# Optimization experiments

Hardware: AMD Instinct MI355X
Metric: run time of the kernel (lower is better)

## Reference

```python
import jax, jax.numpy as jnp
import numpy as np

C = 256  # in_channels
B, N = 8, 2048


def setup_inputs() -> dict:
    key = jax.random.key(0)
    ks = jax.random.split(key, 9)
    s = 1.0 / np.sqrt(C)  # conv1d default init scale (approx)
    return {
        "x": jax.random.normal(ks[0], (B, C, N), jnp.float32),
        "wq": jax.random.normal(ks[1], (C, C), jnp.float32) * s,
        "bq": jax.random.normal(ks[2], (C,), jnp.float32) * s,
        "wk": jax.random.normal(ks[3], (C, C), jnp.float32) * s,
        "bk": jax.random.normal(ks[4], (C,), jnp.float32) * s,
        "wv": jax.random.normal(ks[5], (C, C), jnp.float32) * s,
        "bv": jax.random.normal(ks[6], (C,), jnp.float32) * s,
        "wo": jax.random.normal(ks[7], (C, C), jnp.float32) * s,
        "bo": jax.random.normal(ks[8], (C,), jnp.float32) * s,
    }


def reference(x, wq, bq, wk, bk, wv, bv, wo, bo):
    # 1x1 Conv1d == channel-wise linear: [C_out,C_in] x [B,C_in,N] -> [B,C_out,N]
    proj = lambda w, b, t: jnp.einsum('ci,bin->bcn', w, t) + b[None, :, None]
    q = proj(wq, bq, x)
    k = proj(wk, bk, x)
    v = proj(wv, bv, x)
    norm = 1.0 / (x.shape[1] ** 0.5)
    # scores: w[b,n,m] = sum_c q[b,c,n] k[b,c,m]
    w = jnp.einsum('bcn,bcm->bnm', q, k) * norm
    w = jax.nn.softmax(w, axis=2)
    # attn output: sum_m v[b,c,m] w[b,n,m] -> [B,C,N]
    av = jnp.einsum('bcm,bnm->bcn', v, w)
    out = proj(wo, bo, av)
    return x + out
```

## Files before the change

### kernel.cpp

```cpp
#include <hip/hip_runtime.h>
#include <hip/hip_bf16.h>

#define CCH 256
#define NSEQ 2048
#define BATCH 8

typedef __hip_bfloat16 bf16;
typedef short s8v __attribute__((ext_vector_type(8)));
typedef float f4v __attribute__((ext_vector_type(4)));
typedef float f16v __attribute__((ext_vector_type(16)));

struct __align__(8) bf16x4 { bf16 v[4]; };

__device__ __forceinline__ float b2f(bf16 h) { return __bfloat162float(h); }
__device__ __forceinline__ bf16 f2b(float f) { return __float2bfloat16(f); }

#define MFMA16(a, b, c) __builtin_amdgcn_mfma_f32_16x16x32_bf16((a), (b), (c), 0, 0, 0)
#define MFMA32(a, b, c) __builtin_amdgcn_mfma_f32_32x32x16_bf16((a), (b), (c), 0, 0, 0)

__device__ __forceinline__ void gload_lds16(const bf16* g, bf16* l) {
    __builtin_amdgcn_global_load_lds(
        (const __attribute__((address_space(1))) unsigned int*)(g),
        (__attribute__((address_space(3))) unsigned int*)(l), 16, 0, 0);
}

__global__ __launch_bounds__(256) void prepw_kernel(
    const float* __restrict__ wq, const float* __restrict__ wk,
    const float* __restrict__ wv, const float* __restrict__ wo,
    bf16* __restrict__ wqb, bf16* __restrict__ wkb,
    bf16* __restrict__ wvb, bf16* __restrict__ wob)
{
    int base = (blockIdx.x * 256 + threadIdx.x) * 8;
    int mat = base >> 16, off = base & 65535;
    const float* s = (mat == 0) ? wq : (mat == 1) ? wk : (mat == 2) ? wv : wo;
    bf16* d = (mat == 0) ? wqb : (mat == 1) ? wkb : (mat == 2) ? wvb : wob;
    int doff = (mat == 3) ? off : (off ^ (((off >> 8) & 7) << 3));
    bf16 tmp[8];
    #pragma unroll
    for (int j = 0; j < 8; ++j) tmp[j] = f2b(s[off + j]);
    *(s8v*)&d[doff] = *(const s8v*)tmp;
}

__global__ __launch_bounds__(512, 6) void qkvprep_kernel(
    const float* __restrict__ x,
    const bf16* __restrict__ Wq, const bf16* __restrict__ Wk,
    const bf16* __restrict__ Wv,
    const float* __restrict__ bq, const float* __restrict__ bk,
    const float* __restrict__ bv,
    bf16* __restrict__ qTt, bf16* __restrict__ kTt, bf16* __restrict__ Vt)
{
    __shared__ bf16 xs[64][260];
    __shared__ bf16 wbuf[2][2][4096];

    const int tile = blockIdx.x;
    const int flat0 = tile * 64;
    const int phase = blockIdx.y;
    const int b = flat0 >> 11, nn = flat0 & 2047;
    const int tid = threadIdx.x;
    const int w = tid >> 6, lane = tid & 63;
    const int l15 = lane & 15, quad = lane >> 4;
    const int ng = w & 3;
    const int ch = w >> 2;
    const float* xb = x + (size_t)b * CCH * NSEQ;

    bf16* qt = qTt + (size_t)tile * 16384;
    bf16* kt = kTt + (size_t)tile * 16384;
    bf16* Vtb = Vt + (size_t)b * CCH * NSEQ;

    const bf16* Wm = (phase == 0) ? Wq : (phase == 1) ? Wk : Wv;
    auto stage = [&](int j, int par) {
        const bf16* src = Wm + (size_t)(ch * 8 + j) * 4096;
        bf16* dst = &wbuf[ch][par][0];
        int seg = (w & 3) * 2;
        gload_lds16(src + (seg + 0) * 512 + lane * 8, dst + (seg + 0) * 512);
        gload_lds16(src + (seg + 1) * 512 + lane * 8, dst + (seg + 1) * 512);
    };

    stage(0, 0);
    #pragma unroll
    for (int i = 0; i < 8; ++i) {
        int f4i = i * 512 + tid;
        int c = f4i >> 4, nq = f4i & 15;
        float4 v4 = *(const float4*)&xb[(size_t)c * NSEQ + nn + nq * 4];
        xs[nq * 4 + 0][c] = f2b(v4.x);
        xs[nq * 4 + 1][c] = f2b(v4.y);
        xs[nq * 4 + 2][c] = f2b(v4.z);
        xs[nq * 4 + 3][c] = f2b(v4.w);
    }
    __syncthreads();

    s8v xf[8];
    #pragma unroll
    for (int t = 0; t < 8; ++t)
        xf[t] = *(const s8v*)&xs[ng * 16 + l15][t * 32 + quad * 8];

    int par = 0;
    #pragma unroll
    for (int j = 0; j < 8; ++j) {
        if (j < 7) stage(j + 1, par ^ 1);

        const char* wb = (const char*)&wbuf[ch][par][0];
        s8v wf[8];
        #pragma unroll
        for (int t = 0; t < 8; ++t)
            wf[t] = *(const s8v*)(wb + l15 * 512 +
                                  ((t * 64 + quad * 16) ^ ((l15 & 7) << 4)));

        const int cs = ch * 8 + j;
        if (phase < 2) {
            f4v a0 = {}, a1 = {};
            #pragma unroll
            for (int t = 0; t < 4; ++t) {
                a0 = MFMA16(wf[t], xf[t], a0);
                a1 = MFMA16(wf[t + 4], xf[t + 4], a1);
            }
            const bool isq = (phase == 0);
            const float* bm = isq ? bq : bk;
            bf16* ot = isq ? qt : kt;
            const float sc = isq ? 0.0625f : 1.0f;
            float4 bb4 = *(const float4*)&bm[cs * 16 + quad * 4];
            float bbr[4] = { bb4.x, bb4.y, bb4.z, bb4.w };
            bf16x4 pk;
            #pragma unroll
            for (int r = 0; r < 4; ++r)
                pk.v[r] = f2b((a0[r] + a1[r] + bbr[r]) * sc);
            int nl = ng * 16 + l15;
            *(bf16x4*)&ot[(cs * 2 + (quad >> 1)) * 512 + nl * 8 + (quad & 1) * 4] = pk;
        } else {
            f4v a0 = {}, a1 = {};
            #pragma unroll
            for (int t = 0; t < 4; ++t) {
                a0 = MFMA16(xf[t], wf[t], a0);
                a1 = MFMA16(xf[t + 4], wf[t + 4], a1);
            }
            int c = cs * 16 + l15;
            float bb = bv[c];
            bf16x4 pk;
            #pragma unroll
            for (int r = 0; r < 4; ++r)
                pk.v[r] = f2b(a0[r] + a1[r] + bb);
            const int m16 = (nn >> 4) + ng;
            size_t e0 = ((size_t)m16 * 256 + c) * 16 + (quad >> 1) * 8 + (quad & 1) * 4;
            *(bf16x4*)&Vtb[e0] = pk;
        }
        __syncthreads();
        par ^= 1;
    }
}

__global__ __launch_bounds__(256, 2) void flash_kernel(
    const bf16* __restrict__ qTt, const bf16* __restrict__ kTt,
    const bf16* __restrict__ Vt, bf16* __restrict__ Opart,
    float* __restrict__ lpart)
{
    __shared__ bf16 Kc[16384];
    __shared__ bf16 Ps[64][68];
    __shared__ float l_s[2][64];

    const int b = blockIdx.x, nt = blockIdx.y, ms = blockIdx.z;
    const int tid = threadIdx.x;
    const int W = tid >> 6, lane = tid & 63;
    const int l31 = lane & 31, h = lane >> 5;
    const int ng = W >> 1, mg = W & 1;
    const int mb = ms * 16;
    const bf16* Vtb = Vt + (size_t)b * CCH * NSEQ;

    s8v qf[16];
    {
        const bf16* qt = qTt + (size_t)(b * 32 + nt) * 16384;
        #pragma unroll
        for (int t = 0; t < 16; ++t)
            qf[t] = *(const s8v*)&qt[(t * 2 + h) * 512 + (ng * 32 + l31) * 8];
    }
    const bf16* vbase = Vtb + (size_t)(W * 64 + l31) * 16 + h * 8;

    f16v O[2][2] = {};
    float lsum = 0.f;

    auto stageK = [&](int a) {
        const bf16* kt = kTt + (size_t)(b * 32 + a) * 16384;
        #pragma unroll
        for (int i = 0; i < 8; ++i) {
            int ch = W * 8 + i;
            gload_lds16(kt + ch * 512 + lane * 8, &Kc[ch * 512]);
        }
    };

    stageK(mb);
    __syncthreads();

    for (int mt = 0; mt < 16; ++mt) {
        f16v S0 = {}, S1 = {};
        __builtin_amdgcn_s_setprio(1);
        #pragma unroll
        for (int t = 0; t < 8; ++t) {
            s8v kf0 = *(const s8v*)&Kc[(t * 2 + h) * 512 + (mg * 32 + l31) * 8];
            s8v kf1 = *(const s8v*)&Kc[((t + 8) * 2 + h) * 512 + (mg * 32 + l31) * 8];
            S0 = MFMA32(kf0, qf[t], S0);
            S1 = MFMA32(kf1, qf[t + 8], S1);
        }
        __builtin_amdgcn_s_setprio(0);
        s8v vf[2][4];
        #pragma unroll
        for (int ks = 0; ks < 4; ++ks)
            #pragma unroll
            for (int cr = 0; cr < 2; ++cr)
                vf[cr][ks] = *(const s8v*)(vbase
                    + (size_t)((mb + mt) * 4 + ks) * 4096 + cr * 512);
        #pragma unroll
        for (int q = 0; q < 4; ++q) {
            bf16x4 pk;
            #pragma unroll
            for (int r = 0; r < 4; ++r) {
                float e = __expf(fminf(S0[q * 4 + r] + S1[q * 4 + r], 60.f));
                lsum += e;
                pk.v[r] = f2b(e);
            }
            *(bf16x4*)&Ps[ng * 32 + l31][mg * 32 + q * 8 + h * 4] = pk;
        }
        __syncthreads();

        if (mt < 15) stageK(mb + mt + 1);

        __builtin_amdgcn_s_setprio(1);
        #pragma unroll
        for (int ks = 0; ks < 4; ++ks) {
            s8v pf0 = *(const s8v*)&Ps[l31][ks * 16 + h * 8];
            s8v pf1 = *(const s8v*)&Ps[32 + l31][ks * 16 + h * 8];
            O[0][0] = MFMA32(vf[0][ks], pf0, O[0][0]);
            O[0][1] = MFMA32(vf[0][ks], pf1, O[0][1]);
            O[1][0] = MFMA32(vf[1][ks], pf0, O[1][0]);
            O[1][1] = MFMA32(vf[1][ks], pf1, O[1][1]);
        }
        __builtin_amdgcn_s_setprio(0);
        __syncthreads();
    }

    {
        float s = lsum + __shfl_xor(lsum, 32);
        if (h == 0) l_s[mg][ng * 32 + l31] = s;
    }
    __syncthreads();
    const size_t pb = (size_t)(b * 32 + nt) * 2 + ms;
    if (tid < 64) lpart[pb * 64 + tid] = l_s[0][tid] + l_s[1][tid];

    bf16* Ob = Opart + pb * 16384;
    #pragma unroll
    for (int cr = 0; cr < 2; ++cr)
        #pragma unroll
        for (int g2 = 0; g2 < 2; ++g2) {
            int n = g2 * 32 + l31;
            #pragma unroll
            for (int q2 = 0; q2 < 4; ++q2) {
                bf16x4 pk;
                #pragma unroll
                for (int j = 0; j < 4; ++j) pk.v[j] = f2b(O[cr][g2][q2 * 4 + j]);
                int c = W * 64 + cr * 32 + q2 * 8 + 4 * h;
                *(bf16x4*)&Ob[(size_t)n * 256 + c] = pk;
            }
        }
}

__global__ __launch_bounds__(512, 4) void outproj_kernel(
    const bf16* __restrict__ Opart, const float* __restrict__ lpart,
    const bf16* __restrict__ Wob, const float* __restrict__ bo,
    const float* __restrict__ x, float* __restrict__ out)
{
    __shared__ bf16 avs[64][260];
    __shared__ float ils[64];

    const int bx = blockIdx.x;
    const int flat0 = bx * 64;
    const int c0 = blockIdx.y * 128;
    const int tid = threadIdx.x;
    const int w = tid >> 6, lane = tid & 63;
    const int l15 = lane & 15, quad = lane >> 4;

    if (tid < 64)
        ils[tid] = 1.f / (lpart[(size_t)(bx * 2) * 64 + tid]
                        + lpart[(size_t)(bx * 2 + 1) * 64 + tid]);
    __syncthreads();

    const bf16x4* O0 = (const bf16x4*)(Opart + (size_t)(bx * 2) * 16384);
    const bf16x4* O1 = O0 + 4096;
    #pragma unroll
    for (int i = 0; i < 8; ++i) {
        int u = i * 512 + tid;
        int n = u >> 6;
        bf16x4 a = O0[u], bb = O1[u];
        float il = ils[n];
        bf16x4 o;
        #pragma unroll
        for (int t = 0; t < 4; ++t)
            o.v[t] = f2b((b2f(a.v[t]) + b2f(bb.v[t])) * il);
        *(bf16x4*)&avs[n][(u & 63) * 4] = o;
    }
    __syncthreads();

    const int bidx = flat0 >> 11, nn = flat0 & 2047;
    const size_t base = (size_t)bidx * CCH * NSEQ;
    const int cg = c0 + w * 16;

    s8v af[8];
    #pragma unroll
    for (int t = 0; t < 8; ++t)
        af[t] = *(const s8v*)&Wob[(size_t)(cg + l15) * CCH + t * 32 + quad * 8];

    f4v O[4] = {};
    #pragma unroll
    for (int nt = 0; nt < 4; ++nt)
        #pragma unroll
        for (int t = 0; t < 8; ++t) {
            s8v br = *(const s8v*)&avs[nt * 16 + l15][t * 32 + quad * 8];
            O[nt] = MFMA16(af[t], br, O[nt]);
        }
    #pragma unroll
    for (int r = 0; r < 4; ++r) {
        int c = cg + quad * 4 + r;
        float bb = bo[c];
        #pragma unroll
        for (int nt = 0; nt < 4; ++nt) {
            size_t idx = base + (size_t)c * NSEQ + nn + nt * 16 + l15;
            out[idx] = O[nt][r] + bb + x[idx];
        }
    }
}

extern "C" void kernel_launch(void* const* d_in, const int* in_sizes, int n_in,
                              void* d_out, int out_size, void* d_ws, size_t ws_size,
                              hipStream_t stream) {
    (void)in_sizes; (void)n_in; (void)out_size; (void)ws_size;
    const float* x  = (const float*)d_in[0];
    const float* wq = (const float*)d_in[1];
    const float* bq = (const float*)d_in[2];
    const float* wk = (const float*)d_in[3];
    const float* bk = (const float*)d_in[4];
    const float* wv = (const float*)d_in[5];
    const float* bv = (const float*)d_in[6];
    const float* wo = (const float*)d_in[7];
    const float* bo = (const float*)d_in[8];
    float* out = (float*)d_out;

    const size_t T = (size_t)BATCH * CCH * NSEQ;
    bf16* qTt  = (bf16*)d_ws;
    bf16* kTt  = qTt + T;
    bf16* Vt   = kTt + T;
    bf16* wqb  = Vt + T;
    bf16* wkb  = wqb + 65536;
    bf16* wvb  = wkb + 65536;
    bf16* wob  = wvb + 65536;
    float* lpart = (float*)(wob + 65536);
    bf16* Opart  = (bf16*)(lpart + 32768);

    prepw_kernel<<<128, 256, 0, stream>>>(wq, wk, wv, wo, wqb, wkb, wvb, wob);
    qkvprep_kernel<<<dim3(256, 3), 512, 0, stream>>>(
        x, wqb, wkb, wvb, bq, bk, bv, qTt, kTt, Vt);
    flash_kernel<<<dim3(8, 32, 2), 256, 0, stream>>>(qTt, kTt, Vt, Opart, lpart);
    outproj_kernel<<<dim3(256, 2), 512, 0, stream>>>(Opart, lpart, wob, bo, x, out);
}
```

Baseline: 156.8 us.

## Fuse output projection into flash kernel and drop split-M partials

The flash attention kernel now handles the full key range per block with 512 threads. Two key tiles are processed per iteration by different wave groups, and partial sums are combined in shared memory. The output projection, bias and residual add are done inside the same kernel, so the separate outproj kernel and the Opart/lpart round-trip through global memory go away. In exchange the grid shrinks from 512 to 256 blocks, each with more LDS, which may lower occupancy and parallelism.

```diff
diff --git a/kernel.cpp b/kernel.cpp
--- a/kernel.cpp
+++ b/kernel.cpp
@@ -148,65 +148,70 @@
     }
 }
 
-__global__ __launch_bounds__(256, 2) void flash_kernel(
+__global__ __launch_bounds__(512, 2) void flash_kernel(
     const bf16* __restrict__ qTt, const bf16* __restrict__ kTt,
-    const bf16* __restrict__ Vt, bf16* __restrict__ Opart,
-    float* __restrict__ lpart)
+    const bf16* __restrict__ Vt, const bf16* __restrict__ Wob,
+    const float* __restrict__ bo, const float* __restrict__ x,
+    float* __restrict__ out)
 {
-    __shared__ bf16 Kc[16384];
-    __shared__ bf16 Ps[64][68];
-    __shared__ float l_s[2][64];
-
-    const int b = blockIdx.x, nt = blockIdx.y, ms = blockIdx.z;
+    __shared__ bf16 Kc[2][16384];
+    __shared__ bf16 Ps[2][64][68];
+    __shared__ bf16 avs[64][260];
+    __shared__ float l_s[4][64];
+    __shared__ float ilt[64];
+
+    const int b = blockIdx.x, ntb = blockIdx.y;
     const int tid = threadIdx.x;
     const int W = tid >> 6, lane = tid & 63;
     const int l31 = lane & 31, h = lane >> 5;
-    const int ng = W >> 1, mg = W & 1;
-    const int mb = ms * 16;
+    const int ng = W >> 2, mg = (W >> 1) & 1, mu = W & 1;
     const bf16* Vtb = Vt + (size_t)b * CCH * NSEQ;
 
     s8v qf[16];
     {
-        const bf16* qt = qTt + (size_t)(b * 32 + nt) * 16384;
+        const bf16* qt = qTt + (size_t)(b * 32 + ntb) * 16384;
         #pragma unroll
         for (int t = 0; t < 16; ++t)
             qf[t] = *(const s8v*)&qt[(t * 2 + h) * 512 + (ng * 32 + l31) * 8];
     }
-    const bf16* vbase = Vtb + (size_t)(W * 64 + l31) * 16 + h * 8;
-
-    f16v O[2][2] = {};
+    const bf16* vbase = Vtb + (size_t)(W * 32 + l31) * 16 + h * 8;
+
+    f16v O[2] = {};
     float lsum = 0.f;
 
-    auto stageK = [&](int a) {
-        const bf16* kt = kTt + (size_t)(b * 32 + a) * 16384;
-        #pragma unroll
-        for (int i = 0; i < 8; ++i) {
-            int ch = W * 8 + i;
-            gload_lds16(kt + ch * 512 + lane * 8, &Kc[ch * 512]);
+    auto stageK2 = [&](int t8) {
+        #pragma unroll
+        for (int u = 0; u < 2; ++u) {
+            const bf16* kt = kTt + (size_t)(b * 32 + t8 * 2 + u) * 16384;
+            #pragma unroll
+            for (int i = 0; i < 4; ++i) {
+                int ch = W * 4 + i;
+                gload_lds16(kt + ch * 512 + lane * 8, &Kc[u][ch * 512]);
+            }
         }
     };
 
-    stageK(mb);
-    __syncthreads();
-
-    for (int mt = 0; mt < 16; ++mt) {
+    stageK2(0);
+    __syncthreads();
+
+    for (int t8 = 0; t8 < 16; ++t8) {
         f16v S0 = {}, S1 = {};
         __builtin_amdgcn_s_setprio(1);
         #pragma unroll
         for (int t = 0; t < 8; ++t) {
-            s8v kf0 = *(const s8v*)&Kc[(t * 2 + h) * 512 + (mg * 32 + l31) * 8];
-            s8v kf1 = *(const s8v*)&Kc[((t + 8) * 2 + h) * 512 + (mg * 32 + l31) * 8];
+            s8v kf0 = *(const s8v*)&Kc[mu][(t * 2 + h) * 512 + (mg * 32 + l31) * 8];
+            s8v kf1 = *(const s8v*)&Kc[mu][((t + 8) * 2 + h) * 512 + (mg * 32 + l31) * 8];
             S0 = MFMA32(kf0, qf[t], S0);
             S1 = MFMA32(kf1, qf[t + 8], S1);
         }
         __builtin_amdgcn_s_setprio(0);
         s8v vf[2][4];
         #pragma unroll
-        for (int ks = 0; ks < 4; ++ks)
-            #pragma unroll
-            for (int cr = 0; cr < 2; ++cr)
-                vf[cr][ks] = *(const s8v*)(vbase
-                    + (size_t)((mb + mt) * 4 + ks) * 4096 + cr * 512);
+        for (int u = 0; u < 2; ++u)
+            #pragma unroll
+            for (int ks = 0; ks < 4; ++ks)
+                vf[u][ks] = *(const s8v*)(vbase
+                    + (size_t)((t8 * 2 + u) * 4 + ks) * 4096);
         #pragma unroll
         for (int q = 0; q < 4; ++q) {
             bf16x4 pk;
@@ -216,112 +221,77 @@
                 lsum += e;
                 pk.v[r] = f2b(e);
             }
-            *(bf16x4*)&Ps[ng * 32 + l31][mg * 32 + q * 8 + h * 4] = pk;
+            *(bf16x4*)&Ps[mu][ng * 32 + l31][mg * 32 + q * 8 + h * 4] = pk;
         }
         __syncthreads();
 
-        if (mt < 15) stageK(mb + mt + 1);
+        if (t8 < 15) stageK2(t8 + 1);
 
         __builtin_amdgcn_s_setprio(1);
         #pragma unroll
-        for (int ks = 0; ks < 4; ++ks) {
-            s8v pf0 = *(const s8v*)&Ps[l31][ks * 16 + h * 8];
-            s8v pf1 = *(const s8v*)&Ps[32 + l31][ks * 16 + h * 8];
-            O[0][0] = MFMA32(vf[0][ks], pf0, O[0][0]);
-            O[0][1] = MFMA32(vf[0][ks], pf1, O[0][1]);
-            O[1][0] = MFMA32(vf[1][ks], pf0, O[1][0]);
-            O[1][1] = MFMA32(vf[1][ks], pf1, O[1][1]);
-        }
+        for (int u = 0; u < 2; ++u)
+            #pragma unroll
+            for (int ks = 0; ks < 4; ++ks) {
+                s8v pf0 = *(const s8v*)&Ps[u][l31][ks * 16 + h * 8];
+                s8v pf1 = *(const s8v*)&Ps[u][32 + l31][ks * 16 + h * 8];
+                O[0] = MFMA32(vf[u][ks], pf0, O[0]);
+                O[1] = MFMA32(vf[u][ks], pf1, O[1]);
+            }
         __builtin_amdgcn_s_setprio(0);
         __syncthreads();
     }
 
     {
         float s = lsum + __shfl_xor(lsum, 32);
-        if (h == 0) l_s[mg][ng * 32 + l31] = s;
-    }
-    __syncthreads();
-    const size_t pb = (size_t)(b * 32 + nt) * 2 + ms;
-    if (tid < 64) lpart[pb * 64 + tid] = l_s[0][tid] + l_s[1][tid];
-
-    bf16* Ob = Opart + pb * 16384;
-    #pragma unroll
-    for (int cr = 0; cr < 2; ++cr)
-        #pragma unroll
-        for (int g2 = 0; g2 < 2; ++g2) {
-            int n = g2 * 32 + l31;
-            #pragma unroll
-            for (int q2 = 0; q2 < 4; ++q2) {
-                bf16x4 pk;
-                #pragma unroll
-                for (int j = 0; j < 4; ++j) pk.v[j] = f2b(O[cr][g2][q2 * 4 + j]);
-                int c = W * 64 + cr * 32 + q2 * 8 + 4 * h;
-                *(bf16x4*)&Ob[(size_t)n * 256 + c] = pk;
-            }
-        }
-}
-
-__global__ __launch_bounds__(512, 4) void outproj_kernel(
-    const bf16* __restrict__ Opart, const float* __restrict__ lpart,
-    const bf16* __restrict__ Wob, const float* __restrict__ bo,
-    const float* __restrict__ x, float* __restrict__ out)
-{
-    __shared__ bf16 avs[64][260];
-    __shared__ float ils[64];
-
-    const int bx = blockIdx.x;
-    const int flat0 = bx * 64;
-    const int c0 = blockIdx.y * 128;
-    const int tid = threadIdx.x;
-    const int w = tid >> 6, lane = tid & 63;
+        if (h == 0) l_s[mg * 2 + mu][ng * 32 + l31] = s;
+    }
+    __syncthreads();
+    if (tid < 64)
+        ilt[tid] = 1.f / (l_s[0][tid] + l_s[1][tid]
+                        + l_s[2][tid] + l_s[3][tid]);
+    __syncthreads();
+
+    #pragma unroll
+    for (int g2 = 0; g2 < 2; ++g2) {
+        float il = ilt[g2 * 32 + l31];
+        #pragma unroll
+        for (int q2 = 0; q2 < 4; ++q2) {
+            bf16x4 pk;
+            #pragma unroll
+            for (int r = 0; r < 4; ++r)
+                pk.v[r] = f2b(O[g2][q2 * 4 + r] * il);
+            *(bf16x4*)&avs[g2 * 32 + l31][W * 32 + q2 * 8 + 4 * h] = pk;
+        }
+    }
+    __syncthreads();
+
     const int l15 = lane & 15, quad = lane >> 4;
-
-    if (tid < 64)
-        ils[tid] = 1.f / (lpart[(size_t)(bx * 2) * 64 + tid]
-                        + lpart[(size_t)(bx * 2 + 1) * 64 + tid]);
-    __syncthreads();
-
-    const bf16x4* O0 = (const bf16x4*)(Opart + (size_t)(bx * 2) * 16384);
-    const bf16x4* O1 = O0 + 4096;
-    #pragma unroll
-    for (int i = 0; i < 8; ++i) {
-        int u = i * 512 + tid;
-        int n = u >> 6;
-        bf16x4 a = O0[u], bb = O1[u];
-        float il = ils[n];
-        bf16x4 o;
-        #pragma unroll
-        for (int t = 0; t < 4; ++t)
-            o.v[t] = f2b((b2f(a.v[t]) + b2f(bb.v[t])) * il);
-        *(bf16x4*)&avs[n][(u & 63) * 4] = o;
-    }
-    __syncthreads();
-
-    const int bidx = flat0 >> 11, nn = flat0 & 2047;
-    const size_t base = (size_t)bidx * CCH * NSEQ;
-    const int cg = c0 + w * 16;
-
-    s8v af[8];
-    #pragma unroll
-    for (int t = 0; t < 8; ++t)
-        af[t] = *(const s8v*)&Wob[(size_t)(cg + l15) * CCH + t * 32 + quad * 8];
-
-    f4v O[4] = {};
-    #pragma unroll
-    for (int nt = 0; nt < 4; ++nt)
-        #pragma unroll
-        for (int t = 0; t < 8; ++t) {
-            s8v br = *(const s8v*)&avs[nt * 16 + l15][t * 32 + quad * 8];
-            O[nt] = MFMA16(af[t], br, O[nt]);
-        }
-    #pragma unroll
-    for (int r = 0; r < 4; ++r) {
-        int c = cg + quad * 4 + r;
-        float bb = bo[c];
-        #pragma unroll
-        for (int nt = 0; nt < 4; ++nt) {
-            size_t idx = base + (size_t)c * NSEQ + nn + nt * 16 + l15;
-            out[idx] = O[nt][r] + bb + x[idx];
+    const int nn = ntb * 64;
+    const size_t base = (size_t)b * CCH * NSEQ;
+    #pragma unroll
+    for (int cs = 0; cs < 2; ++cs) {
+        const int cg = W * 32 + cs * 16;
+        s8v af[8];
+        #pragma unroll
+        for (int t = 0; t < 8; ++t)
+            af[t] = *(const s8v*)&Wob[(size_t)(cg + l15) * CCH + t * 32 + quad * 8];
+        f4v O4[4] = {};
+        #pragma unroll
+        for (int nt2 = 0; nt2 < 4; ++nt2)
+            #pragma unroll
+            for (int t = 0; t < 8; ++t) {
+                s8v br = *(const s8v*)&avs[nt2 * 16 + l15][t * 32 + quad * 8];
+                O4[nt2] = MFMA16(af[t], br, O4[nt2]);
+            }
+        #pragma unroll
+        for (int r = 0; r < 4; ++r) {
+            int c = cg + quad * 4 + r;
+            float bb = bo[c];
+            #pragma unroll
+            for (int nt2 = 0; nt2 < 4; ++nt2) {
+                size_t idx = base + (size_t)c * NSEQ + nn + nt2 * 16 + l15;
+                out[idx] = O4[nt2][r] + bb + x[idx];
+            }
         }
     }
 }
@@ -349,12 +319,10 @@
     bf16* wkb  = wqb + 65536;
     bf16* wvb  = wkb + 65536;
     bf16* wob  = wvb + 65536;
-    float* lpart = (float*)(wob + 65536);
-    bf16* Opart  = (bf16*)(lpart + 32768);
 
     prepw_kernel<<<128, 256, 0, stream>>>(wq, wk, wv, wo, wqb, wkb, wvb, wob);
     qkvprep_kernel<<<dim3(256, 3), 512, 0, stream>>>(
         x, wqb, wkb, wvb, bq, bk, bv, qTt, kTt, Vt);
-    flash_kernel<<<dim3(8, 32, 2), 256, 0, stream>>>(qTt, kTt, Vt, Opart, lpart);
-    outproj_kernel<<<dim3(256, 2), 512, 0, stream>>>(Opart, lpart, wob, bo, x, out);
-}
+    flash_kernel<<<dim3(8, 32), 512, 0, stream>>>(
+        qTt, kTt, Vt, wob, bo, x, out);
+}
```

After: 156.7 us. About the same (-0.1%).

## Make QKV projection persistent with full weight matrix resident in LDS

Applied to the files above, without the earlier changes.

The QKV projection kernel now loads the whole 256x256 bf16 weight matrix into LDS once per block. Each block then loops over 8 tiles of 32 positions instead of streaming weight slices per 64-position tile. The grid drops from 256x3 to 64x3 blocks, so the weight matrix is fetched from global memory far fewer times. The cost is 128KB of LDS per block, which limits occupancy to one block per CU, and fewer blocks in flight to hide the x loads.

```diff
diff --git a/kernel.cpp b/kernel.cpp
--- a/kernel.cpp
+++ b/kernel.cpp
@@ -41,7 +41,7 @@
     *(s8v*)&d[doff] = *(const s8v*)tmp;
 }
 
-__global__ __launch_bounds__(512, 6) void qkvprep_kernel(
+__global__ __launch_bounds__(512, 2) void qkvprep_kernel(
     const float* __restrict__ x,
     const bf16* __restrict__ Wq, const bf16* __restrict__ Wk,
     const bf16* __restrict__ Wv,
@@ -49,102 +49,104 @@
     const float* __restrict__ bv,
     bf16* __restrict__ qTt, bf16* __restrict__ kTt, bf16* __restrict__ Vt)
 {
-    __shared__ bf16 xs[64][260];
-    __shared__ bf16 wbuf[2][2][4096];
-
-    const int tile = blockIdx.x;
-    const int flat0 = tile * 64;
-    const int phase = blockIdx.y;
-    const int b = flat0 >> 11, nn = flat0 & 2047;
+    __shared__ bf16 wlds[65536];
+    __shared__ bf16 xs[32][260];
+
+    const int mat = blockIdx.y;
+    const int bx = blockIdx.x;
     const int tid = threadIdx.x;
     const int w = tid >> 6, lane = tid & 63;
     const int l15 = lane & 15, quad = lane >> 4;
-    const int ng = w & 3;
-    const int ch = w >> 2;
-    const float* xb = x + (size_t)b * CCH * NSEQ;
-
-    bf16* qt = qTt + (size_t)tile * 16384;
-    bf16* kt = kTt + (size_t)tile * 16384;
-    bf16* Vtb = Vt + (size_t)b * CCH * NSEQ;
-
-    const bf16* Wm = (phase == 0) ? Wq : (phase == 1) ? Wk : Wv;
-    auto stage = [&](int j, int par) {
-        const bf16* src = Wm + (size_t)(ch * 8 + j) * 4096;
-        bf16* dst = &wbuf[ch][par][0];
-        int seg = (w & 3) * 2;
-        gload_lds16(src + (seg + 0) * 512 + lane * 8, dst + (seg + 0) * 512);
-        gload_lds16(src + (seg + 1) * 512 + lane * 8, dst + (seg + 1) * 512);
-    };
-
-    stage(0, 0);
-    #pragma unroll
-    for (int i = 0; i < 8; ++i) {
-        int f4i = i * 512 + tid;
-        int c = f4i >> 4, nq = f4i & 15;
-        float4 v4 = *(const float4*)&xb[(size_t)c * NSEQ + nn + nq * 4];
-        xs[nq * 4 + 0][c] = f2b(v4.x);
-        xs[nq * 4 + 1][c] = f2b(v4.y);
-        xs[nq * 4 + 2][c] = f2b(v4.z);
-        xs[nq * 4 + 3][c] = f2b(v4.w);
-    }
-    __syncthreads();
-
-    s8v xf[8];
-    #pragma unroll
-    for (int t = 0; t < 8; ++t)
-        xf[t] = *(const s8v*)&xs[ng * 16 + l15][t * 32 + quad * 8];
-
-    int par = 0;
-    #pragma unroll
-    for (int j = 0; j < 8; ++j) {
-        if (j < 7) stage(j + 1, par ^ 1);
-
-        const char* wb = (const char*)&wbuf[ch][par][0];
-        s8v wf[8];
+    const int ng = w & 1;
+    const int cs0 = (w >> 1) * 4;
+
+    const bf16* Wm = (mat == 0) ? Wq : (mat == 1) ? Wk : Wv;
+    const float* bm = (mat == 0) ? bq : (mat == 1) ? bk : bv;
+    const float sc = (mat == 0) ? 0.0625f : 1.0f;
+
+    #pragma unroll
+    for (int i = 0; i < 16; ++i) {
+        int kb = w * 16 + i;
+        gload_lds16(Wm + kb * 512 + lane * 8, &wlds[kb * 512]);
+    }
+
+    for (int it = 0; it < 8; ++it) {
+        const int t32 = it * 64 + bx;
+        const int b = t32 >> 6;
+        const int nn = (t32 & 63) * 32;
+        const float* xb = x + (size_t)b * CCH * NSEQ;
+
+        float4 v4[4];
+        #pragma unroll
+        for (int i = 0; i < 4; ++i) {
+            int f4i = i * 512 + tid;
+            int c = f4i >> 3, nq = f4i & 7;
+            v4[i] = *(const float4*)&xb[(size_t)c * NSEQ + nn + nq * 4];
+        }
+        __syncthreads();
+        #pragma unroll
+        for (int i = 0; i < 4; ++i) {
+            int f4i = i * 512 + tid;
+            int c = f4i >> 3, nq = f4i & 7;
+            xs[nq * 4 + 0][c] = f2b(v4[i].x);
+            xs[nq * 4 + 1][c] = f2b(v4[i].y);
+            xs[nq * 4 + 2][c] = f2b(v4[i].z);
+            xs[nq * 4 + 3][c] = f2b(v4[i].w);
+        }
+        __syncthreads();
+
+        s8v xf[8];
         #pragma unroll
         for (int t = 0; t < 8; ++t)
-            wf[t] = *(const s8v*)(wb + l15 * 512 +
-                                  ((t * 64 + quad * 16) ^ ((l15 & 7) << 4)));
-
-        const int cs = ch * 8 + j;
-        if (phase < 2) {
-            f4v a0 = {}, a1 = {};
+            xf[t] = *(const s8v*)&xs[ng * 16 + l15][t * 32 + quad * 8];
+
+        const char* wb = (const char*)wlds;
+        #pragma unroll
+        for (int k = 0; k < 4; ++k) {
+            const int cs = cs0 + k;
+            s8v wf[8];
             #pragma unroll
-            for (int t = 0; t < 4; ++t) {
-                a0 = MFMA16(wf[t], xf[t], a0);
-                a1 = MFMA16(wf[t + 4], xf[t + 4], a1);
+            for (int t = 0; t < 8; ++t)
+                wf[t] = *(const s8v*)(wb + (cs * 16 + l15) * 512 +
+                              ((t * 64 + quad * 16) ^ ((l15 & 7) << 4)));
+
+            if (mat < 2) {
+                f4v a0 = {}, a1 = {};
+                #pragma unroll
+                for (int t = 0; t < 4; ++t) {
+                    a0 = MFMA16(wf[t], xf[t], a0);
+                    a1 = MFMA16(wf[t + 4], xf[t + 4], a1);
+                }
+                float4 bb4 = *(const float4*)&bm[cs * 16 + quad * 4];
+                float bbr[4] = { bb4.x, bb4.y, bb4.z, bb4.w };
+                bf16x4 pk;
+                #pragma unroll
+                for (int r = 0; r < 4; ++r)
+                    pk.v[r] = f2b((a0[r] + a1[r] + bbr[r]) * sc);
+                bf16* ot = (mat == 0 ? qTt : kTt)
+                         + (size_t)(b * 32 + ((t32 & 63) >> 1)) * 16384;
+                int nl = (t32 & 1) * 32 + ng * 16 + l15;
+                *(bf16x4*)&ot[(cs * 2 + (quad >> 1)) * 512 + nl * 8 + (quad & 1) * 4] = pk;
+            } else {
+                f4v a0 = {}, a1 = {};
+                #pragma unroll
+                for (int t = 0; t < 4; ++t) {
+                    a0 = MFMA16(xf[t], wf[t], a0);
+                    a1 = MFMA16(xf[t + 4], wf[t + 4], a1);
+                }
+                int c = cs * 16 + l15;
+                float bb = bm[c];
+                bf16x4 pk;
+                #pragma unroll
+                for (int r = 0; r < 4; ++r)
+                    pk.v[r] = f2b(a0[r] + a1[r] + bb);
+                bf16* Vtb = Vt + (size_t)b * CCH * NSEQ;
+                const int m16 = (t32 & 63) * 2 + ng;
+                size_t e0 = ((size_t)m16 * 256 + c) * 16
+                          + (quad >> 1) * 8 + (quad & 1) * 4;
+                *(bf16x4*)&Vtb[e0] = pk;
             }
-            const bool isq = (phase == 0);
-            const float* bm = isq ? bq : bk;
-            bf16* ot = isq ? qt : kt;
-            const float sc = isq ? 0.0625f : 1.0f;
-            float4 bb4 = *(const float4*)&bm[cs * 16 + quad * 4];
-            float bbr[4] = { bb4.x, bb4.y, bb4.z, bb4.w };
-            bf16x4 pk;
-            #pragma unroll
-            for (int r = 0; r < 4; ++r)
-                pk.v[r] = f2b((a0[r] + a1[r] + bbr[r]) * sc);
-            int nl = ng * 16 + l15;
-            *(bf16x4*)&ot[(cs * 2 + (quad >> 1)) * 512 + nl * 8 + (quad & 1) * 4] = pk;
-        } else {
-            f4v a0 = {}, a1 = {};
-            #pragma unroll
-            for (int t = 0; t < 4; ++t) {
-                a0 = MFMA16(xf[t], wf[t], a0);
-                a1 = MFMA16(xf[t + 4], wf[t + 4], a1);
-            }
-            int c = cs * 16 + l15;
-            float bb = bv[c];
-            bf16x4 pk;
-            #pragma unroll
-            for (int r = 0; r < 4; ++r)
-                pk.v[r] = f2b(a0[r] + a1[r] + bb);
-            const int m16 = (nn >> 4) + ng;
-            size_t e0 = ((size_t)m16 * 256 + c) * 16 + (quad >> 1) * 8 + (quad & 1) * 4;
-            *(bf16x4*)&Vtb[e0] = pk;
-        }
-        __syncthreads();
-        par ^= 1;
+        }
     }
 }
 
@@ -353,7 +355,7 @@
     bf16* Opart  = (bf16*)(lpart + 32768);
 
     prepw_kernel<<<128, 256, 0, stream>>>(wq, wk, wv, wo, wqb, wkb, wvb, wob);
-    qkvprep_kernel<<<dim3(256, 3), 512, 0, stream>>>(
+    qkvprep_kernel<<<dim3(64, 3), 512, 0, stream>>>(
         x, wqb, wkb, wvb, bq, bk, bv, qTt, kTt, Vt);
     flash_kernel<<<dim3(8, 32, 2), 256, 0, stream>>>(qTt, kTt, Vt, Opart, lpart);
     outproj_kernel<<<dim3(256, 2), 512, 0, stream>>>(Opart, lpart, wob, bo, x, out);
```

New measurement: 167.3 us. 1.07x slower.
